# Kernel optimization log

Hardware: AMD Instinct MI355X
Metric: run time of the kernel (lower is better)

The kernel has to match this reference:

```python
import jax, jax.numpy as jnp
import numpy as np

B, L, D = 2, 1024, 768
N_LAYERS, D_STATE, D_CONV, EXPAND = 4, 16, 4, 2
D_INNER = EXPAND * D
DT_RANK = (D + 15) // 16  # 48, ceil(d_model/16) as in reference Mamba
N_CLS = 10
EPS = 1e-6


def rmsnorm(x, w):
    return x * jax.lax.rsqrt(jnp.mean(x * x, axis=-1, keepdims=True) + EPS) * w


def mamba_block(x, in_w, conv_w, conv_b, xp_w, dt_w, dt_b, A_log, D_skip, out_w):
    # x: (B, L, D)
    Bsz = x.shape[0]
    xz = jnp.einsum('bld,ed->ble', x, in_w)            # (B, L, 2*d_inner)
    xi, z = jnp.split(xz, 2, axis=-1)
    # causal depthwise conv over the sequence dim
    xc = jnp.transpose(xi, (0, 2, 1))                  # (B, d_inner, L)
    xc = jax.lax.conv_general_dilated(
        xc, conv_w[:, None, :], (1,), [(D_CONV - 1, 0)],
        dimension_numbers=('NCH', 'OIH', 'NCH'), feature_group_count=D_INNER)
    xc = jnp.transpose(xc, (0, 2, 1)) + conv_b         # (B, L, d_inner)
    xc = jax.nn.silu(xc)
    # input-dependent SSM parameters
    x_dbl = jnp.einsum('bld,ed->ble', xc, xp_w)        # (B, L, dt_rank + 2*d_state)
    dt, Bs, Cs = jnp.split(x_dbl, [DT_RANK, DT_RANK + D_STATE], axis=-1)
    delta = jax.nn.softplus(jnp.einsum('blr,dr->bld', dt, dt_w) + dt_b)  # (B, L, d_inner)
    A = -jnp.exp(A_log)                                # (d_inner, d_state)
    dA = jnp.exp(delta[..., None] * A)                 # (B, L, d_inner, d_state)
    dBu = delta[..., None] * Bs[:, :, None, :] * xc[..., None]

    def step(h, inp):
        dA_t, dBu_t, C_t = inp
        h = dA_t * h + dBu_t                           # (B, d_inner, d_state)
        y = jnp.einsum('bdn,bn->bd', h, C_t)
        return h, y

    h0 = jnp.zeros((Bsz, D_INNER, D_STATE), x.dtype)
    _, ys = jax.lax.scan(step, h0, (jnp.swapaxes(dA, 0, 1),
                                    jnp.swapaxes(dBu, 0, 1),
                                    jnp.swapaxes(Cs, 0, 1)))
    y = jnp.swapaxes(ys, 0, 1) + xc * D_skip           # (B, L, d_inner)
    y = y * jax.nn.silu(z)                             # gate
    return jnp.einsum('bld,od->blo', y, out_w)


def reference(x, norm_w, in_proj_w, conv_w, conv_b, x_proj_w, dt_proj_w, dt_proj_b,
              A_log, D_skip, out_proj_w, final_norm_w,
              head1_w, head1_b, head_norm_w, head2_w, head2_b):
    for i in range(N_LAYERS):
        res = x
        x = rmsnorm(x, norm_w[i])
        x = mamba_block(x, in_proj_w[i], conv_w[i], conv_b[i], x_proj_w[i],
                        dt_proj_w[i], dt_proj_b[i], A_log[i], D_skip[i],
                        out_proj_w[i]) + res
    x = rmsnorm(x, final_norm_w)
    last = x[:, -1, :]                                 # (B, D)
    h = last @ head1_w.T + head1_b
    h = rmsnorm(h, head_norm_w)
    h = jax.nn.gelu(h, approximate=False)              # torch nn.GELU default is exact erf
    return h @ head2_w.T + head2_b                     # (B, N_CLS)


def setup_inputs() -> dict:
    key = jax.random.key(0)
    ks = jax.random.split(key, 10)
    s = 0.02
    x = jax.random.normal(ks[0], (B, L, D), jnp.float32)
    norm_w = jnp.ones((N_LAYERS, D), jnp.float32)
    in_proj_w = s * jax.random.normal(ks[1], (N_LAYERS, 2 * D_INNER, D), jnp.float32)
    conv_w = s * jax.random.normal(ks[2], (N_LAYERS, D_INNER, D_CONV), jnp.float32)
    conv_b = jnp.zeros((N_LAYERS, D_INNER), jnp.float32)
    x_proj_w = s * jax.random.normal(ks[3], (N_LAYERS, DT_RANK + 2 * D_STATE, D_INNER), jnp.float32)
    dt_proj_w = s * jax.random.normal(ks[4], (N_LAYERS, D_INNER, DT_RANK), jnp.float32)
    dt_proj_b = jnp.full((N_LAYERS, D_INNER), -4.6, jnp.float32)  # softplus(-4.6) ~ 0.01
    A_log = jnp.log(jnp.broadcast_to(
        jnp.arange(1, D_STATE + 1, dtype=jnp.float32), (N_LAYERS, D_INNER, D_STATE)) + 0.0)
    D_skip = jnp.ones((N_LAYERS, D_INNER), jnp.float32)
    out_proj_w = s * jax.random.normal(ks[5], (N_LAYERS, D, D_INNER), jnp.float32)
    final_norm_w = jnp.ones((D,), jnp.float32)
    head1_w = s * jax.random.normal(ks[6], (D, D), jnp.float32)
    head1_b = jnp.zeros((D,), jnp.float32)
    head_norm_w = jnp.ones((D,), jnp.float32)
    head2_w = s * jax.random.normal(ks[7], (N_CLS, D), jnp.float32)
    head2_b = jnp.zeros((N_CLS,), jnp.float32)
    return {"x": x, "norm_w": norm_w, "in_proj_w": in_proj_w, "conv_w": conv_w,
            "conv_b": conv_b, "x_proj_w": x_proj_w, "dt_proj_w": dt_proj_w,
            "dt_proj_b": dt_proj_b, "A_log": A_log, "D_skip": D_skip,
            "out_proj_w": out_proj_w, "final_norm_w": final_norm_w,
            "head1_w": head1_w, "head1_b": head1_b, "head_norm_w": head_norm_w,
            "head2_w": head2_w, "head2_b": head2_b}
```

## Files before the change

kernel.cpp:

```cpp
#include <hip/hip_runtime.h>
#include <hip/hip_bf16.h>
#include <math.h>

typedef __bf16 bf16;
typedef __bf16 bf16x4 __attribute__((ext_vector_type(4)));
typedef __bf16 bf16x8 __attribute__((ext_vector_type(8)));
typedef float floatx4 __attribute__((ext_vector_type(4)));

#define BB 2
#define LL 1024
#define DD 768
#define DI 1536
#define MROWS 2048
#define NXP 80
#define DTRANK 48
#define DTPAD 64
#define DSTATE 16
#define NC 16
#define CLEN 64
#define KSPLIT 16
#define OPKS 4
#define LOG2E 1.4426950408889634f
#define LN2   0.6931471805599453f
#define TROW 132
#define SYROW 68

__device__ __forceinline__ void ld16(void* lds, const void* g) {
    __builtin_amdgcn_global_load_lds(
        (const __attribute__((address_space(1))) void*)g,
        (__attribute__((address_space(3))) void*)lds, 16, 0, 0);
}

__device__ __forceinline__ void wait_vm0() {
    asm volatile("s_waitcnt vmcnt(0)" ::: "memory");
}

__device__ __forceinline__ float row16_sum(float x) {
    float t;
    t = __int_as_float(__builtin_amdgcn_update_dpp(0, __float_as_int(x), 0x111, 0xF, 0xF, true)); x += t;
    t = __int_as_float(__builtin_amdgcn_update_dpp(0, __float_as_int(x), 0x112, 0xF, 0xF, true)); x += t;
    t = __int_as_float(__builtin_amdgcn_update_dpp(0, __float_as_int(x), 0x114, 0xF, 0xF, true)); x += t;
    t = __int_as_float(__builtin_amdgcn_update_dpp(0, __float_as_int(x), 0x118, 0xF, 0xF, true)); x += t;
    return x;
}

__device__ __forceinline__ float exp2_raw(float x) {
#if __has_builtin(__builtin_amdgcn_exp2f)
    return __builtin_amdgcn_exp2f(x);
#else
    float r; asm("v_exp_f32 %0, %1" : "=v"(r) : "v"(x)); return r;
#endif
}
__device__ __forceinline__ float log2_raw(float x) {
#if __has_builtin(__builtin_amdgcn_logf)
    return __builtin_amdgcn_logf(x);
#else
    float r; asm("v_log_f32 %0, %1" : "=v"(r) : "v"(x)); return r;
#endif
}
__device__ __forceinline__ float softplus_fast(float v) {
    float t  = exp2_raw(v * LOG2E);
    float sp = log2_raw(1.f + t) * LN2;
    return (v > 20.f) ? v : sp;
}

#define N1 (4 * 3072 * 768)
#define N2 (4 * NXP * DI)
#define N3 (4 * DI * DTPAD)
#define N4 (4 * DD * DI)
#define N5 (4 * DSTATE * DI)
__global__ __launch_bounds__(256) void cvt_all_k(const float* __restrict__ in_proj_w,
                                                 const float* __restrict__ x_proj_w,
                                                 const float* __restrict__ dt_proj_w,
                                                 const float* __restrict__ out_proj_w,
                                                 const float* __restrict__ A_log,
                                                 bf16* __restrict__ w_in,
                                                 bf16* __restrict__ w_xp,
                                                 bf16* __restrict__ w_dt,
                                                 bf16* __restrict__ w_out,
                                                 float* __restrict__ a2T) {
    int i = blockIdx.x * 256 + threadIdx.x;
    if (i < N1) { w_in[i] = (bf16)in_proj_w[i]; return; }
    i -= N1;
    if (i < N2) { w_xp[i] = (bf16)x_proj_w[i]; return; }
    i -= N2;
    if (i < N3) {
        int row = i >> 6, c = i & 63;
        w_dt[i] = (c < DTRANK) ? (bf16)dt_proj_w[row * DTRANK + c] : (bf16)0.f;
        return;
    }
    i -= N3;
    if (i < N4) { w_out[i] = (bf16)out_proj_w[i]; return; }
    i -= N4;
    if (i < N5) {
        int layer = i / (DSTATE * DI);
        int rem   = i - layer * (DSTATE * DI);
        int n     = rem / DI;
        int d     = rem - n * DI;
        a2T[i] = -__expf(A_log[(size_t)layer * DI * DSTATE + d * DSTATE + n]) * LOG2E;
    }
}

__global__ __launch_bounds__(256) void rmsnorm_k(const float* __restrict__ x,
                                                 const float* __restrict__ w,
                                                 bf16* __restrict__ out) {
    int row = blockIdx.x;
    const float* xr = x + (size_t)row * DD;
    int tid = threadIdx.x;
    float v[3]; float ss = 0.f;
    for (int j = 0; j < 3; j++) { v[j] = xr[tid + j * 256]; ss += v[j] * v[j]; }
    for (int o = 1; o < 64; o <<= 1) ss += __shfl_xor(ss, o, 64);
    __shared__ float sred[4];
    if ((tid & 63) == 0) sred[tid >> 6] = ss;
    __syncthreads();
    float scale = rsqrtf((sred[0] + sred[1] + sred[2] + sred[3]) / (float)DD + 1e-6f);
    for (int j = 0; j < 3; j++) {
        int c = tid + j * 256;
        out[(size_t)row * DD + c] = (bf16)(v[j] * scale * w[c]);
    }
}

template <int MODE>
__global__ __launch_bounds__(256) void gemm_bt(const bf16* __restrict__ A,
                                               const bf16* __restrict__ W,
                                               float* __restrict__ Cf,
                                               bf16* __restrict__ Cb,
                                               int M, int N, int K) {
    __shared__ bf16 As[128][32];
    __shared__ bf16 Ws[128][32];
    const int tid  = threadIdx.x;
    const int m0   = blockIdx.x * 128;
    const int n0   = blockIdx.y * 128;
    const int wave = tid >> 6;
    const int lane = tid & 63;
    const int wm   = (wave >> 1) * 64;
    const int wn   = (wave & 1) * 64;
    const int lrow = lane & 15;
    const int quad = lane >> 4;

    int kbeg = 0, kend = K;
    if constexpr (MODE == 5) {
        int kseg = K / gridDim.z;
        kbeg = blockIdx.z * kseg;
        kend = kbeg + kseg;
        Cf  += (size_t)blockIdx.z * M * N;
    }

    floatx4 acc[4][4];
    for (int mi = 0; mi < 4; mi++)
        for (int ni = 0; ni < 4; ni++) acc[mi][ni] = (floatx4){0.f, 0.f, 0.f, 0.f};

    const int r0  = tid >> 2;
    const int r1  = r0 + 64;
    const int seg = (tid & 3) * 8;
    char* asb0 = (char*)As + wave * 1024;
    char* asb1 = (char*)As + 4096 + wave * 1024;
    char* wsb0 = (char*)Ws + wave * 1024;
    char* wsb1 = (char*)Ws + 4096 + wave * 1024;

    for (int kb = kbeg; kb < kend; kb += 32) {
        int gk = kb + seg;
        __syncthreads();
        ld16(asb0, A + (size_t)(m0 + r0) * K + gk);
        ld16(asb1, A + (size_t)(m0 + r1) * K + gk);
        ld16(wsb0, W + (size_t)(n0 + r0) * K + gk);
        ld16(wsb1, W + (size_t)(n0 + r1) * K + gk);
        wait_vm0();
        __syncthreads();
        bf16x8 af[4], wf[4];
        for (int mi = 0; mi < 4; mi++) af[mi] = *(const bf16x8*)&As[wm + mi * 16 + lrow][quad * 8];
        for (int ni = 0; ni < 4; ni++) wf[ni] = *(const bf16x8*)&Ws[wn + ni * 16 + lrow][quad * 8];
        for (int mi = 0; mi < 4; mi++)
            for (int ni = 0; ni < 4; ni++)
                acc[mi][ni] = __builtin_amdgcn_mfma_f32_16x16x32_bf16(af[mi], wf[ni], acc[mi][ni], 0, 0, 0);
    }
    for (int mi = 0; mi < 4; mi++) {
        int rowb = m0 + wm + mi * 16 + quad * 4;
        for (int ni = 0; ni < 4; ni++) {
            int col = n0 + wn + ni * 16 + lrow;
            for (int r = 0; r < 4; r++) {
                int row = rowb + r;
                float v = acc[mi][ni][r];
                if constexpr (MODE == 1) Cb[(size_t)row * N + col] = (bf16)v;
                else                     Cf[(size_t)row * N + col] = v;
            }
        }
    }
}

__global__ __launch_bounds__(256) void op_reduce_norm_k(const float* __restrict__ part,
                                                        const float* __restrict__ resid,
                                                        const float* __restrict__ nw,
                                                        float* __restrict__ xout,
                                                        bf16* __restrict__ xnb) {
    int row = blockIdx.x;
    int tid = threadIdx.x;
    float v[3]; float ss = 0.f;
    for (int j = 0; j < 3; j++) {
        int c = tid + j * 256;
        size_t idx = (size_t)row * DD + c;
        float s = resid[idx];
        for (int ks = 0; ks < OPKS; ks++) s += part[(size_t)ks * MROWS * DD + idx];
        v[j] = s;
        xout[idx] = s;
        ss += s * s;
    }
    for (int o = 1; o < 64; o <<= 1) ss += __shfl_xor(ss, o, 64);
    __shared__ float sred[4];
    if ((tid & 63) == 0) sred[tid >> 6] = ss;
    __syncthreads();
    float scale = rsqrtf((sred[0] + sred[1] + sred[2] + sred[3]) / (float)DD + 1e-6f);
    for (int j = 0; j < 3; j++) {
        int c = tid + j * 256;
        xnb[(size_t)row * DD + c] = (bf16)(v[j] * scale * nw[c]);
    }
}

__global__ __launch_bounds__(256) void gemm_xp(const bf16* __restrict__ A,
                                               const bf16* __restrict__ W,
                                               float* __restrict__ part) {
    __shared__ bf16 As[64][40];
    __shared__ bf16 Ws[128][40];
    const int tid  = threadIdx.x;
    const int m0   = blockIdx.x * 64;
    const int ks   = blockIdx.y;
    const int k0   = ks * (DI / KSPLIT);
    const int wave = tid >> 6;
    const int lane = tid & 63;
    const int lrow = lane & 15;
    const int quad = lane >> 4;
    const int wm   = wave * 16;

    floatx4 acc[5];
    for (int ni = 0; ni < 5; ni++) acc[ni] = (floatx4){0.f, 0.f, 0.f, 0.f};

    const int ra  = tid >> 2;
    const int rw1 = ra + 64;
    const int seg = (tid & 3) * 8;

    for (int kb = 0; kb < DI / KSPLIT; kb += 32) {
        int gk = k0 + kb + seg;
        bf16x8 va = *(const bf16x8*)(A + (size_t)(m0 + ra) * DI + gk);
        bf16x8 vw0, vw1;
        if (ra < NXP) vw0 = *(const bf16x8*)(W + (size_t)ra * DI + gk);
        else          for (int j = 0; j < 8; j++) vw0[j] = (bf16)0.f;
        if (rw1 < NXP) vw1 = *(const bf16x8*)(W + (size_t)rw1 * DI + gk);
        else           for (int j = 0; j < 8; j++) vw1[j] = (bf16)0.f;
        __syncthreads();
        *(bf16x8*)&As[ra][seg]  = va;
        *(bf16x8*)&Ws[ra][seg]  = vw0;
        *(bf16x8*)&Ws[rw1][seg] = vw1;
        __syncthreads();
        bf16x8 af = *(const bf16x8*)&As[wm + lrow][quad * 8];
        for (int ni = 0; ni < 5; ni++) {
            bf16x8 wf = *(const bf16x8*)&Ws[ni * 16 + lrow][quad * 8];
            acc[ni] = __builtin_amdgcn_mfma_f32_16x16x32_bf16(af, wf, acc[ni], 0, 0, 0);
        }
    }
    float* pout = part + (size_t)ks * MROWS * NXP;
    for (int ni = 0; ni < 5; ni++) {
        int col = ni * 16 + lrow;
        for (int r = 0; r < 4; r++) {
            int row = m0 + wm + quad * 4 + r;
            pout[(size_t)row * NXP + col] = acc[ni][r];
        }
    }
}

__global__ __launch_bounds__(256) void xp_reduce_k(const float* __restrict__ part,
                                                   float* __restrict__ xdbl,
                                                   bf16* __restrict__ dtbf) {
    int idx = blockIdx.x * 256 + threadIdx.x;
    if (idx >= MROWS * NXP) return;
    float s = 0.f;
    for (int j = 0; j < KSPLIT; j++) s += part[(size_t)j * MROWS * NXP + idx];
    xdbl[idx] = s;
    int m = idx / NXP, c = idx - m * NXP;
    if (c < DTRANK)      dtbf[m * DTPAD + c] = (bf16)s;
    else if (c < DTPAD)  dtbf[m * DTPAD + c] = (bf16)0.f;
}

__global__ __launch_bounds__(256) void conv_silu_k(const bf16* __restrict__ xz,
                                                   const float* __restrict__ cw,
                                                   const float* __restrict__ cb,
                                                   bf16* __restrict__ xcb,
                                                   bf16* __restrict__ gzb) {
    int t = blockIdx.x * 256 + threadIdx.x;
    if (t >= MROWS * (DI / 4)) return;
    int m = t / (DI / 4);
    int d = (t - m * (DI / 4)) * 4;
    int l = m & (LL - 1);
    float acc[4];
    floatx4 cwv[4];
    for (int q = 0; q < 4; q++) {
        acc[q] = cb[d + q];
        cwv[q] = *(const floatx4*)&cw[(d + q) * 4];
    }
    for (int k = 0; k < 4; k++) {
        int lp = l - 3 + k;
        if (lp >= 0) {
            bf16x4 v = *(const bf16x4*)&xz[(size_t)(m - 3 + k) * (2 * DI) + d];
            for (int q = 0; q < 4; q++) acc[q] += (float)v[q] * cwv[q][k];
        }
    }
    bf16x4 xo, go;
    bf16x4 z4 = *(const bf16x4*)&xz[(size_t)m * (2 * DI) + DI + d];
    for (int q = 0; q < 4; q++) {
        float s = acc[q] / (1.f + __expf(-acc[q]));
        xo[q] = (bf16)s;
        float zv = (float)z4[q];
        go[q] = (bf16)(zv / (1.f + __expf(-zv)));
    }
    *(bf16x4*)&xcb[(size_t)m * DI + d] = xo;
    *(bf16x4*)&gzb[(size_t)m * DI + d] = go;
}

__global__ __launch_bounds__(256) void scanA_k(const bf16* __restrict__ dtb,
                                               const bf16* __restrict__ wdt,
                                               const float* __restrict__ dtbias,
                                               const bf16* __restrict__ xcb,
                                               const float* __restrict__ xdbl,
                                               const float* __restrict__ A_log,
                                               float* __restrict__ Pbuf,
                                               float* __restrict__ Sbuf,
                                               float2* __restrict__ ylsc) {
    const int b   = blockIdx.y;
    const int d0  = blockIdx.x * 16;
    const int c   = blockIdx.z;
    const int tid = threadIdx.x;
    const int dl  = tid >> 4;
    const int n   = tid & 15;
    const int wv  = tid >> 6;
    const int lane = tid & 63;
    const int lr  = lane & 15;
    const int q   = lane >> 4;
    const int l0  = c * CLEN;

    const float a2 = -__expf(A_log[(size_t)(d0 + dl) * DSTATE + n]) * LOG2E;
    const float bi = dtbias[d0 + lr];

    __shared__ __align__(16) bf16  sxc[CLEN][16];
    __shared__ __align__(16) float sdpT[16][TROW];
    __shared__ __align__(16) float sbcT[16][TROW];
    __shared__ __align__(16) float syT[16][SYROW];
    __shared__ __align__(16) float sST[16][SYROW];

    const bf16x8 wf0 = *(const bf16x8*)&wdt[(size_t)(d0 + lr) * DTPAD + q * 8];
    const bf16x8 wf1 = *(const bf16x8*)&wdt[(size_t)(d0 + lr) * DTPAD + 32 + q * 8];

    bf16x8 a0, a1;
    {
        const bf16* r = &dtb[(size_t)(b * LL + l0 + 16 * wv + lr) * DTPAD + q * 8];
        a0 = *(const bf16x8*)r;
        a1 = *(const bf16x8*)(r + 32);
    }
    float Bv[4], Cv[4];
    #pragma unroll
    for (int k2 = 0; k2 < 4; ++k2) {
        int ii = (tid + 256 * k2) >> 4;
        const float* p = &xdbl[(size_t)(b * LL + l0 + ii) * NXP + DTRANK + n];
        Bv[k2] = p[0];
        Cv[k2] = p[DSTATE];
    }
    if (tid < 128) {
        int r2 = tid >> 1, c2 = tid & 1;
        ld16((char*)&sxc[0][0] + (tid & ~63) * 16,
             xcb + (size_t)(b * LL + l0 + r2) * DI + d0 + c2 * 8);
    }
    wait_vm0();
    __syncthreads();

    {
        floatx4 dacc = (floatx4){0.f, 0.f, 0.f, 0.f};
        dacc = __builtin_amdgcn_mfma_f32_16x16x32_bf16(a0, wf0, dacc, 0, 0, 0);
        dacc = __builtin_amdgcn_mfma_f32_16x16x32_bf16(a1, wf1, dacc, 0, 0, 0);
        float vv[4], xvv[4];
        #pragma unroll
        for (int r = 0; r < 4; ++r) {
            int l = 16 * wv + q * 4 + r;
            vv[r]  = softplus_fast(dacc[r] + bi);
            xvv[r] = (float)sxc[l][lr];
        }
        int L0 = 16 * wv + q * 4;
        *(float4*)&sdpT[lr][2 * L0] =
            make_float4(vv[0], vv[0] * xvv[0], vv[1], vv[1] * xvv[1]);
        *(float4*)&sdpT[lr][2 * L0 + 4] =
            make_float4(vv[2], vv[2] * xvv[2], vv[3], vv[3] * xvv[3]);
        #pragma unroll
        for (int k2 = 0; k2 < 4; ++k2) {
            int ii = (tid + 256 * k2) >> 4;
            *(float2*)&sbcT[n][2 * ii] = make_float2(Bv[k2], Cv[k2]);
        }
    }
    __syncthreads();

    {
        float h = 0.f, sdc = 0.f;
        const float4* dpr = (const float4*)&sdpT[dl][0];
        const float4* bcr = (const float4*)&sbcT[n][0];
        float4 dA[4], bA[4], dB2[4], bB2[4];
        float y4[4], s4[4];
        #pragma unroll
        for (int t = 0; t < 4; ++t) { dA[t] = dpr[t]; bA[t] = bcr[t]; }
        #pragma unroll
        for (int g = 0; g < 8; ++g) {
            #pragma unroll
            for (int t = 0; t < 4; ++t) {
                if (g + 1 < 8) {
                    if ((g & 1) == 0) { dB2[t] = dpr[(g + 1) * 4 + t]; bB2[t] = bcr[(g + 1) * 4 + t]; }
                    else              { dA[t]  = dpr[(g + 1) * 4 + t]; bA[t]  = bcr[(g + 1) * 4 + t]; }
                }
            }
            #pragma unroll
            for (int i = 0; i < 8; ++i) {
                float4 v = ((g & 1) == 0) ? dA[i >> 1] : dB2[i >> 1];
                float4 w = ((g & 1) == 0) ? bA[i >> 1] : bB2[i >> 1];
                float dvx = (i & 1) ? v.z : v.x;
                float dpy = (i & 1) ? v.w : v.y;
                float bx  = (i & 1) ? w.z : w.x;
                float cy  = (i & 1) ? w.w : w.y;
                float e = exp2_raw(dvx * a2);
                h = __builtin_fmaf(e, h, dpy * bx);
                sdc += dvx;
                y4[i & 3] = row16_sum(h * cy);
                s4[i & 3] = sdc;
                if ((i & 3) == 3 && n == 0) {
                    *(floatx4*)&syT[dl][g * 8 + i - 3] =
                        (floatx4){y4[0], y4[1], y4[2], y4[3]};
                    *(floatx4*)&sST[dl][g * 8 + i - 3] =
                        (floatx4){s4[0], s4[1], s4[2], s4[3]};
                }
            }
        }
        size_t o = (((size_t)c * BB + b) * DI + (d0 + dl)) * DSTATE + n;
        Pbuf[o] = exp2_raw(a2 * sdc);
        Sbuf[o] = h;
    }
    __syncthreads();

    #pragma unroll
    for (int k2 = 0; k2 < 4; ++k2) {
        int idx = tid + 256 * k2, ii = idx >> 4, dd = idx & 15;
        ylsc[(size_t)(b * LL + l0 + ii) * DI + d0 + dd] =
            make_float2(syT[dd][ii], sST[dd][ii]);
    }
}

__global__ __launch_bounds__(256) void compose_k(const float* __restrict__ P,
                                                 const float* __restrict__ S,
                                                 float* __restrict__ H0T) {
    int idx = blockIdx.x * 256 + threadIdx.x;
    const size_t stride = (size_t)BB * DI * DSTATE;
    int b = idx / (DI * DSTATE);
    int rest = idx - b * (DI * DSTATE);
    int d = rest >> 4;
    int n = rest & 15;
    float h = 0.f;
    #pragma unroll
    for (int c = 0; c < NC; ++c) {
        H0T[((size_t)c * BB + b) * (DSTATE * DI) + (size_t)n * DI + d] = h;
        h = __builtin_fmaf(P[(size_t)c * stride + idx], h, S[(size_t)c * stride + idx]);
    }
}

__global__ __launch_bounds__(256) void corr_k(const float2* __restrict__ ylsc,
                                              const float* __restrict__ xdbl,
                                              const float* __restrict__ H0T,
                                              const float* __restrict__ a2T,
                                              const bf16* __restrict__ xcb,
                                              const bf16* __restrict__ gzb,
                                              const float* __restrict__ Dskip,
                                              bf16* __restrict__ ybf) {
    const int b = blockIdx.y, c = blockIdx.z;
    const int tid = threadIdx.x;
    const int t6 = blockIdx.x * 256 + tid;
    const int dq   = (t6 % 384) * 4;
    const int loff = t6 / 384;

    __shared__ __align__(16) float sC[CLEN][16];
    {
        int l = tid >> 2, nn = (tid & 3) * 4;
        *(float4*)&sC[l][nn] =
            *(const float4*)&xdbl[(size_t)(b * LL + c * CLEN + l) * NXP + DTRANK + DSTATE + nn];
    }
    __syncthreads();

    const float* h0base = H0T + ((size_t)c * BB + b) * (DSTATE * DI);
    int m0_ = b * LL + c * CLEN + loff;
    floatx4 acc[4];
    float4 sc[4];
    #pragma unroll
    for (int s = 0; s < 4; ++s) {
        size_t mo = (size_t)(m0_ + s * 16) * DI + dq;
        float4 u0 = *(const float4*)&ylsc[mo];
        float4 u1 = *(const float4*)&ylsc[mo + 2];
        acc[s] = (floatx4){u0.x, u0.z, u1.x, u1.z};
        sc[s]  = make_float4(u0.y, u0.w, u1.y, u1.w);
    }
    #pragma unroll
    for (int n = 0; n < DSTATE; ++n) {
        float4 a2v = *(const float4*)&a2T[(size_t)n * DI + dq];
        float4 h0v = *(const float4*)&h0base[(size_t)n * DI + dq];
        #pragma unroll
        for (int s = 0; s < 4; ++s) {
            float Cn = sC[loff + s * 16][n];
            acc[s][0] = __builtin_fmaf(Cn * h0v.x, exp2_raw(a2v.x * sc[s].x), acc[s][0]);
            acc[s][1] = __builtin_fmaf(Cn * h0v.y, exp2_raw(a2v.y * sc[s].y), acc[s][1]);
            acc[s][2] = __builtin_fmaf(Cn * h0v.z, exp2_raw(a2v.z * sc[s].z), acc[s][2]);
            acc[s][3] = __builtin_fmaf(Cn * h0v.w, exp2_raw(a2v.w * sc[s].w), acc[s][3]);
        }
    }
    float4 Dsk = *(const float4*)&Dskip[dq];
    #pragma unroll
    for (int s = 0; s < 4; ++s) {
        size_t mo = (size_t)(m0_ + s * 16) * DI + dq;
        bf16x4 xc4 = *(const bf16x4*)&xcb[mo];
        bf16x4 gz4 = *(const bf16x4*)&gzb[mo];
        bf16x4 yo;
        yo[0] = (bf16)((acc[s][0] + (float)xc4[0] * Dsk.x) * (float)gz4[0]);
        yo[1] = (bf16)((acc[s][1] + (float)xc4[1] * Dsk.y) * (float)gz4[1]);
        yo[2] = (bf16)((acc[s][2] + (float)xc4[2] * Dsk.z) * (float)gz4[2]);
        yo[3] = (bf16)((acc[s][3] + (float)xc4[3] * Dsk.w) * (float)gz4[3]);
        *(bf16x4*)&ybf[mo] = yo;
    }
}

__global__ __launch_bounds__(256) void head_norm_k(const float* __restrict__ x,
                                                   const float* __restrict__ fnw,
                                                   float* __restrict__ xn_buf) {
    int b = blockIdx.x;
    int tid = threadIdx.x;
    const float* xr = x + ((size_t)b * LL + (LL - 1)) * DD;
    __shared__ float sred[4];
    float v[3]; float ss = 0.f;
    for (int j = 0; j < 3; j++) { v[j] = xr[tid + j * 256]; ss += v[j] * v[j]; }
    for (int o = 1; o < 64; o <<= 1) ss += __shfl_xor(ss, o, 64);
    if ((tid & 63) == 0) sred[tid >> 6] = ss;
    __syncthreads();
    float scale = rsqrtf((sred[0] + sred[1] + sred[2] + sred[3]) / (float)DD + 1e-6f);
    for (int j = 0; j < 3; j++) {
        int c = tid + j * 256;
        xn_buf[(size_t)b * DD + c] = v[j] * scale * fnw[c];
    }
}

__global__ __launch_bounds__(256) void head_h1_k(const float* __restrict__ xn_buf,
                                                 const float* __restrict__ h1w,
                                                 const float* __restrict__ h1b,
                                                 float* __restrict__ h_buf) {
    int b  = blockIdx.x;
    int o0 = blockIdx.y * 64;
    int tid = threadIdx.x;
    __shared__ float sx[DD];
    for (int c = tid; c < DD; c += 256) sx[c] = xn_buf[(size_t)b * DD + c];
    __syncthreads();
    int wave = tid >> 6, lane = tid & 63;
    for (int j = 0; j < 16; j++) {
        int o = o0 + wave * 16 + j;
        const float* wrow = h1w + (size_t)o * DD;
        float acc = 0.f;
        for (int k = 0; k < 12; k++) {
            int c = lane + 64 * k;
            acc += wrow[c] * sx[c];
        }
        for (int off = 1; off < 64; off <<= 1) acc += __shfl_xor(acc, off, 64);
        if (lane == 0) h_buf[(size_t)b * DD + o] = acc + h1b[o];
    }
}

__global__ __launch_bounds__(256) void head_out_k(const float* __restrict__ h_buf,
                                                  const float* __restrict__ hnw,
                                                  const float* __restrict__ h2w,
                                                  const float* __restrict__ h2b,
                                                  float* __restrict__ out) {
    int b = blockIdx.x;
    int tid = threadIdx.x;
    __shared__ float hh[DD];
    __shared__ float sred[4];
    const float* hr = h_buf + (size_t)b * DD;
    float ss = 0.f;
    for (int c = tid; c < DD; c += 256) { float v = hr[c]; ss += v * v; }
    for (int o = 1; o < 64; o <<= 1) ss += __shfl_xor(ss, o, 64);
    if ((tid & 63) == 0) sred[tid >> 6] = ss;
    __syncthreads();
    float sc = rsqrtf((sred[0] + sred[1] + sred[2] + sred[3]) / (float)DD + 1e-6f);
    for (int c = tid; c < DD; c += 256) {
        float v = hr[c] * sc * hnw[c];
        hh[c] = 0.5f * v * (1.f + erff(v * 0.70710678118f));
    }
    __syncthreads();
    int w = tid >> 6, lane = tid & 63;
    for (int j = w; j < 10; j += 4) {
        float acc = 0.f;
        const float* wrow = h2w + (size_t)j * DD;
        for (int c = lane; c < DD; c += 64) acc += hh[c] * wrow[c];
        for (int o = 1; o < 64; o <<= 1) acc += __shfl_xor(acc, o, 64);
        if (lane == 0) out[b * 10 + j] = acc + h2b[j];
    }
}

extern "C" void kernel_launch(void* const* d_in, const int* in_sizes, int n_in,
                              void* d_out, int out_size, void* d_ws, size_t ws_size,
                              hipStream_t stream) {
    const float* x_in      = (const float*)d_in[0];
    const float* norm_w    = (const float*)d_in[1];
    const float* in_proj_w = (const float*)d_in[2];
    const float* conv_w    = (const float*)d_in[3];
    const float* conv_b    = (const float*)d_in[4];
    const float* x_proj_w  = (const float*)d_in[5];
    const float* dt_proj_w = (const float*)d_in[6];
    const float* dt_proj_b = (const float*)d_in[7];
    const float* A_log     = (const float*)d_in[8];
    const float* D_skip    = (const float*)d_in[9];
    const float* out_proj_w= (const float*)d_in[10];
    const float* fnw       = (const float*)d_in[11];
    const float* h1w       = (const float*)d_in[12];
    const float* h1b       = (const float*)d_in[13];
    const float* hnw       = (const float*)d_in[14];
    const float* h2w       = (const float*)d_in[15];
    const float* h2b       = (const float*)d_in[16];
    float* out = (float*)d_out;

    char* ws = (char*)d_ws;
    size_t off = 0;
    auto alloc = [&](size_t bytes) -> void* {
        void* p = ws + off;
        off += (bytes + 255) & ~(size_t)255;
        return p;
    };
    bf16* w_in  = (bf16*)alloc((size_t)N1 * 2);
    bf16* w_xp  = (bf16*)alloc((size_t)N2 * 2);
    bf16* w_dt  = (bf16*)alloc((size_t)N3 * 2);
    bf16* w_out = (bf16*)alloc((size_t)N4 * 2);
    float* a2T  = (float*)alloc((size_t)N5 * 4);
    bf16* xn_bf = (bf16*)alloc((size_t)MROWS * DD * 2);
    bf16* xz_bf = (bf16*)alloc((size_t)MROWS * 2 * DI * 2);
    bf16* xc_bf = (bf16*)alloc((size_t)MROWS * DI * 2);
    bf16* gz_bf = (bf16*)alloc((size_t)MROWS * DI * 2);
    float* xdbl = (float*)alloc((size_t)MROWS * NXP * 4);
    bf16* dt_bf = (bf16*)alloc((size_t)MROWS * DTPAD * 2);
    bf16* y_bf  = (bf16*)alloc((size_t)MROWS * DI * 2);
    float* x_buf= (float*)alloc((size_t)MROWS * DD * 4);
    float* Pbuf = (float*)alloc((size_t)NC * BB * DI * DSTATE * 4);
    float* Sbuf = (float*)alloc((size_t)NC * BB * DI * DSTATE * 4);
    float* H0T  = (float*)alloc((size_t)NC * BB * DI * DSTATE * 4);
    float2* ylsc= (float2*)alloc((size_t)MROWS * DI * 8);
    float* xnl  = (float*)alloc((size_t)BB * DD * 4);
    float* hbuf = (float*)alloc((size_t)BB * DD * 4);
    float* xp_part = (float*)alloc((size_t)KSPLIT * MROWS * NXP * 4);
    float* op_part = (float*)alloc((size_t)OPKS * MROWS * DD * 4);

    {
        int ntot = N1 + N2 + N3 + N4 + N5;
        cvt_all_k<<<(ntot + 255) / 256, 256, 0, stream>>>(
            in_proj_w, x_proj_w, dt_proj_w, out_proj_w, A_log,
            w_in, w_xp, w_dt, w_out, a2T);
    }

    for (int i = 0; i < 4; i++) {
        const float* x_src = (i == 0) ? x_in : x_buf;
        if (i == 0)
            rmsnorm_k<<<MROWS, 256, 0, stream>>>(x_src, norm_w, xn_bf);
        gemm_bt<1><<<dim3(MROWS / 128, 3072 / 128), 256, 0, stream>>>(
            xn_bf, w_in + (size_t)i * 3072 * 768, nullptr, xz_bf,
            MROWS, 2 * DI, DD);
        conv_silu_k<<<(MROWS * (DI / 4) + 255) / 256, 256, 0, stream>>>(
            xz_bf, conv_w + (size_t)i * DI * 4, conv_b + (size_t)i * DI, xc_bf, gz_bf);
        gemm_xp<<<dim3(MROWS / 64, KSPLIT), 256, 0, stream>>>(
            xc_bf, w_xp + (size_t)i * NXP * DI, xp_part);
        xp_reduce_k<<<(MROWS * NXP + 255) / 256, 256, 0, stream>>>(xp_part, xdbl, dt_bf);
        scanA_k<<<dim3(DI / 16, BB, NC), 256, 0, stream>>>(
            dt_bf, w_dt + (size_t)i * DI * DTPAD, dt_proj_b + (size_t)i * DI,
            xc_bf, xdbl, A_log + (size_t)i * DI * DSTATE, Pbuf, Sbuf, ylsc);
        compose_k<<<(BB * DI * DSTATE) / 256, 256, 0, stream>>>(Pbuf, Sbuf, H0T);
        corr_k<<<dim3(24, BB, NC), 256, 0, stream>>>(
            ylsc, xdbl, H0T, a2T + (size_t)i * DSTATE * DI,
            xc_bf, gz_bf, D_skip + (size_t)i * DI, y_bf);
        gemm_bt<5><<<dim3(MROWS / 128, DD / 128, OPKS), 256, 0, stream>>>(
            y_bf, w_out + (size_t)i * DD * DI, op_part, nullptr,
            MROWS, DD, DI);
        op_reduce_norm_k<<<MROWS, 256, 0, stream>>>(
            op_part, x_src, norm_w + ((i + 1) & 3) * DD, x_buf, xn_bf);
    }

    head_norm_k<<<BB, 256, 0, stream>>>(x_buf, fnw, xnl);
    head_h1_k<<<dim3(BB, DD / 64), 256, 0, stream>>>(xnl, h1w, h1b, hbuf);
    head_out_k<<<BB, 256, 0, stream>>>(hbuf, hnw, h2w, h2b, out);
}
```

Baseline: 626.5 us.

## Restructure chunked scan so each thread owns four states of 64-channel block

The chunk-scan kernel now handles 64 channels per block instead of 16. Each thread keeps four state elements in registers, so the per-step reduction over states needs two DPP shuffles instead of four. The dt projection runs four MFMA tiles per block, and the per-step results are written straight to global memory, which removes the transposed LDS staging and one barrier. The cost is a quarter as many blocks (fewer waves to hide latency), four exp2 calls per thread per step, and scattered 8-byte global stores from one lane in four.

```diff
diff --git a/kernel.cpp b/kernel.cpp
--- a/kernel.cpp
+++ b/kernel.cpp
@@ -18,12 +18,11 @@
 #define DSTATE 16
 #define NC 16
 #define CLEN 64
+#define DBLK 64
 #define KSPLIT 16
 #define OPKS 4
 #define LOG2E 1.4426950408889634f
 #define LN2   0.6931471805599453f
-#define TROW 132
-#define SYROW 68
 
 __device__ __forceinline__ void ld16(void* lds, const void* g) {
     __builtin_amdgcn_global_load_lds(
@@ -35,12 +34,10 @@
     asm volatile("s_waitcnt vmcnt(0)" ::: "memory");
 }
 
-__device__ __forceinline__ float row16_sum(float x) {
+__device__ __forceinline__ float quad4_sum(float x) {
     float t;
-    t = __int_as_float(__builtin_amdgcn_update_dpp(0, __float_as_int(x), 0x111, 0xF, 0xF, true)); x += t;
-    t = __int_as_float(__builtin_amdgcn_update_dpp(0, __float_as_int(x), 0x112, 0xF, 0xF, true)); x += t;
-    t = __int_as_float(__builtin_amdgcn_update_dpp(0, __float_as_int(x), 0x114, 0xF, 0xF, true)); x += t;
-    t = __int_as_float(__builtin_amdgcn_update_dpp(0, __float_as_int(x), 0x118, 0xF, 0xF, true)); x += t;
+    t = __int_as_float(__builtin_amdgcn_update_dpp(0, __float_as_int(x), 0xB1, 0xF, 0xF, true)); x += t;
+    t = __int_as_float(__builtin_amdgcn_update_dpp(0, __float_as_int(x), 0x4E, 0xF, 0xF, true)); x += t;
     return x;
 }
 
@@ -315,7 +312,7 @@
     *(bf16x4*)&gzb[(size_t)m * DI + d] = go;
 }
 
-__global__ __launch_bounds__(256) void scanA_k(const bf16* __restrict__ dtb,
+__global__ __launch_bounds__(256) void scanB_k(const bf16* __restrict__ dtb,
                                                const bf16* __restrict__ wdt,
                                                const float* __restrict__ dtbias,
                                                const bf16* __restrict__ xcb,
@@ -325,124 +322,124 @@
                                                float* __restrict__ Sbuf,
                                                float2* __restrict__ ylsc) {
     const int b   = blockIdx.y;
-    const int d0  = blockIdx.x * 16;
+    const int d0  = blockIdx.x * DBLK;
     const int c   = blockIdx.z;
     const int tid = threadIdx.x;
-    const int dl  = tid >> 4;
-    const int n   = tid & 15;
     const int wv  = tid >> 6;
     const int lane = tid & 63;
     const int lr  = lane & 15;
     const int q   = lane >> 4;
     const int l0  = c * CLEN;
-
-    const float a2 = -__expf(A_log[(size_t)(d0 + dl) * DSTATE + n]) * LOG2E;
-    const float bi = dtbias[d0 + lr];
-
-    __shared__ __align__(16) bf16  sxc[CLEN][16];
-    __shared__ __align__(16) float sdpT[16][TROW];
-    __shared__ __align__(16) float sbcT[16][TROW];
-    __shared__ __align__(16) float syT[16][SYROW];
-    __shared__ __align__(16) float sST[16][SYROW];
-
-    const bf16x8 wf0 = *(const bf16x8*)&wdt[(size_t)(d0 + lr) * DTPAD + q * 8];
-    const bf16x8 wf1 = *(const bf16x8*)&wdt[(size_t)(d0 + lr) * DTPAD + 32 + q * 8];
-
-    bf16x8 a0, a1;
+    const int dl  = tid >> 2;
+    const int nq  = tid & 3;
+
+    __shared__ __align__(16) float sdp[DBLK][68];
+    __shared__ __align__(16) bf16  sxc[CLEN][DBLK];
+    __shared__ __align__(16) float sB[CLEN][20];
+    __shared__ __align__(16) float sC[CLEN][20];
+
     {
-        const bf16* r = &dtb[(size_t)(b * LL + l0 + 16 * wv + lr) * DTPAD + q * 8];
-        a0 = *(const bf16x8*)r;
-        a1 = *(const bf16x8*)(r + 32);
-    }
-    float Bv[4], Cv[4];
-    #pragma unroll
-    for (int k2 = 0; k2 < 4; ++k2) {
-        int ii = (tid + 256 * k2) >> 4;
-        const float* p = &xdbl[(size_t)(b * LL + l0 + ii) * NXP + DTRANK + n];
-        Bv[k2] = p[0];
-        Cv[k2] = p[DSTATE];
-    }
-    if (tid < 128) {
-        int r2 = tid >> 1, c2 = tid & 1;
-        ld16((char*)&sxc[0][0] + (tid & ~63) * 16,
-             xcb + (size_t)(b * LL + l0 + r2) * DI + d0 + c2 * 8);
-    }
-    wait_vm0();
-    __syncthreads();
+        int t2 = tid;
+        ld16((char*)&sxc[0][0] + (t2 & ~63) * 16,
+             xcb + (size_t)(b * LL + l0 + (t2 >> 3)) * DI + d0 + (t2 & 7) * 8);
+        t2 = tid + 256;
+        ld16((char*)&sxc[0][0] + (t2 & ~63) * 16,
+             xcb + (size_t)(b * LL + l0 + (t2 >> 3)) * DI + d0 + (t2 & 7) * 8);
+    }
 
     {
-        floatx4 dacc = (floatx4){0.f, 0.f, 0.f, 0.f};
-        dacc = __builtin_amdgcn_mfma_f32_16x16x32_bf16(a0, wf0, dacc, 0, 0, 0);
-        dacc = __builtin_amdgcn_mfma_f32_16x16x32_bf16(a1, wf1, dacc, 0, 0, 0);
-        float vv[4], xvv[4];
-        #pragma unroll
-        for (int r = 0; r < 4; ++r) {
-            int l = 16 * wv + q * 4 + r;
-            vv[r]  = softplus_fast(dacc[r] + bi);
-            xvv[r] = (float)sxc[l][lr];
-        }
-        int L0 = 16 * wv + q * 4;
-        *(float4*)&sdpT[lr][2 * L0] =
-            make_float4(vv[0], vv[0] * xvv[0], vv[1], vv[1] * xvv[1]);
-        *(float4*)&sdpT[lr][2 * L0 + 4] =
-            make_float4(vv[2], vv[2] * xvv[2], vv[3], vv[3] * xvv[3]);
+        float Bv[4], Cv[4];
         #pragma unroll
         for (int k2 = 0; k2 < 4; ++k2) {
             int ii = (tid + 256 * k2) >> 4;
-            *(float2*)&sbcT[n][2 * ii] = make_float2(Bv[k2], Cv[k2]);
-        }
-    }
-    __syncthreads();
-
+            const float* p = &xdbl[(size_t)(b * LL + l0 + ii) * NXP + DTRANK + (tid & 15)];
+            Bv[k2] = p[0];
+            Cv[k2] = p[DSTATE];
+        }
+        #pragma unroll
+        for (int k2 = 0; k2 < 4; ++k2) {
+            int ii = (tid + 256 * k2) >> 4;
+            sB[ii][tid & 15] = Bv[k2];
+            sC[ii][tid & 15] = Cv[k2];
+        }
+    }
+
+    float4 a2q;
     {
-        float h = 0.f, sdc = 0.f;
-        const float4* dpr = (const float4*)&sdpT[dl][0];
-        const float4* bcr = (const float4*)&sbcT[n][0];
-        float4 dA[4], bA[4], dB2[4], bB2[4];
-        float y4[4], s4[4];
+        float4 al = *(const float4*)&A_log[(size_t)(d0 + dl) * DSTATE + nq * 4];
+        a2q.x = -__expf(al.x) * LOG2E;
+        a2q.y = -__expf(al.y) * LOG2E;
+        a2q.z = -__expf(al.z) * LOG2E;
+        a2q.w = -__expf(al.w) * LOG2E;
+    }
+
+    {
+        const bf16* ar = &dtb[(size_t)(b * LL + l0 + 16 * wv + lr) * DTPAD + q * 8];
+        bf16x8 a0 = *(const bf16x8*)ar;
+        bf16x8 a1 = *(const bf16x8*)(ar + 32);
         #pragma unroll
-        for (int t = 0; t < 4; ++t) { dA[t] = dpr[t]; bA[t] = bcr[t]; }
-        #pragma unroll
-        for (int g = 0; g < 8; ++g) {
+        for (int j = 0; j < 4; ++j) {
+            const bf16* wr = &wdt[(size_t)(d0 + 16 * j + lr) * DTPAD + q * 8];
+            bf16x8 w0 = *(const bf16x8*)wr;
+            bf16x8 w1 = *(const bf16x8*)(wr + 32);
+            floatx4 dacc = (floatx4){0.f, 0.f, 0.f, 0.f};
+            dacc = __builtin_amdgcn_mfma_f32_16x16x32_bf16(a0, w0, dacc, 0, 0, 0);
+            dacc = __builtin_amdgcn_mfma_f32_16x16x32_bf16(a1, w1, dacc, 0, 0, 0);
+            float bi = dtbias[d0 + 16 * j + lr];
             #pragma unroll
-            for (int t = 0; t < 4; ++t) {
-                if (g + 1 < 8) {
-                    if ((g & 1) == 0) { dB2[t] = dpr[(g + 1) * 4 + t]; bB2[t] = bcr[(g + 1) * 4 + t]; }
-                    else              { dA[t]  = dpr[(g + 1) * 4 + t]; bA[t]  = bcr[(g + 1) * 4 + t]; }
-                }
+            for (int r = 0; r < 4; ++r) {
+                int l = 16 * wv + q * 4 + r;
+                sdp[16 * j + lr][l] = softplus_fast(dacc[r] + bi);
             }
+        }
+    }
+
+    wait_vm0();
+    __syncthreads();
+
+    {
+        float4 hq = make_float4(0.f, 0.f, 0.f, 0.f);
+        float sdc = 0.f;
+        const float* dvrow = &sdp[dl][0];
+        const unsigned short* xcp = (const unsigned short*)&sxc[0][0] + dl;
+        for (int g = 0; g < 16; ++g) {
+            float4 dvv = *(const float4*)&dvrow[4 * g];
+            float2 yst[4];
             #pragma unroll
-            for (int i = 0; i < 8; ++i) {
-                float4 v = ((g & 1) == 0) ? dA[i >> 1] : dB2[i >> 1];
-                float4 w = ((g & 1) == 0) ? bA[i >> 1] : bB2[i >> 1];
-                float dvx = (i & 1) ? v.z : v.x;
-                float dpy = (i & 1) ? v.w : v.y;
-                float bx  = (i & 1) ? w.z : w.x;
-                float cy  = (i & 1) ? w.w : w.y;
-                float e = exp2_raw(dvx * a2);
-                h = __builtin_fmaf(e, h, dpy * bx);
-                sdc += dvx;
-                y4[i & 3] = row16_sum(h * cy);
-                s4[i & 3] = sdc;
-                if ((i & 3) == 3 && n == 0) {
-                    *(floatx4*)&syT[dl][g * 8 + i - 3] =
-                        (floatx4){y4[0], y4[1], y4[2], y4[3]};
-                    *(floatx4*)&sST[dl][g * 8 + i - 3] =
-                        (floatx4){s4[0], s4[1], s4[2], s4[3]};
-                }
+            for (int i2 = 0; i2 < 4; ++i2) {
+                int i = 4 * g + i2;
+                float dv = (i2 == 0) ? dvv.x : (i2 == 1) ? dvv.y : (i2 == 2) ? dvv.z : dvv.w;
+                float xcv = __int_as_float((unsigned)xcp[i * DBLK] << 16);
+                float du = dv * xcv;
+                float4 Bq = *(const float4*)&sB[i][4 * nq];
+                float4 Cq = *(const float4*)&sC[i][4 * nq];
+                hq.x = __builtin_fmaf(exp2_raw(a2q.x * dv), hq.x, du * Bq.x);
+                hq.y = __builtin_fmaf(exp2_raw(a2q.y * dv), hq.y, du * Bq.y);
+                hq.z = __builtin_fmaf(exp2_raw(a2q.z * dv), hq.z, du * Bq.z);
+                hq.w = __builtin_fmaf(exp2_raw(a2q.w * dv), hq.w, du * Bq.w);
+                float y = __builtin_fmaf(Cq.w, hq.w,
+                          __builtin_fmaf(Cq.z, hq.z,
+                          __builtin_fmaf(Cq.y, hq.y, Cq.x * hq.x)));
+                y = quad4_sum(y);
+                sdc += dv;
+                yst[i2] = make_float2(y, sdc);
             }
-        }
-        size_t o = (((size_t)c * BB + b) * DI + (d0 + dl)) * DSTATE + n;
-        Pbuf[o] = exp2_raw(a2 * sdc);
-        Sbuf[o] = h;
-    }
-    __syncthreads();
-
-    #pragma unroll
-    for (int k2 = 0; k2 < 4; ++k2) {
-        int idx = tid + 256 * k2, ii = idx >> 4, dd = idx & 15;
-        ylsc[(size_t)(b * LL + l0 + ii) * DI + d0 + dd] =
-            make_float2(syT[dd][ii], sST[dd][ii]);
+            if (nq == 0) {
+                size_t base = (size_t)(b * LL + l0 + 4 * g) * DI + d0 + dl;
+                ylsc[base]          = yst[0];
+                ylsc[base + DI]     = yst[1];
+                ylsc[base + 2 * DI] = yst[2];
+                ylsc[base + 3 * DI] = yst[3];
+            }
+        }
+        float4 Pq;
+        Pq.x = exp2_raw(a2q.x * sdc);
+        Pq.y = exp2_raw(a2q.y * sdc);
+        Pq.z = exp2_raw(a2q.z * sdc);
+        Pq.w = exp2_raw(a2q.w * sdc);
+        size_t o = (((size_t)c * BB + b) * DI + (d0 + dl)) * DSTATE + nq * 4;
+        *(float4*)&Pbuf[o] = Pq;
+        *(float4*)&Sbuf[o] = make_float4(hq.x, hq.y, hq.z, hq.w);
     }
 }
 
@@ -669,7 +666,7 @@
         gemm_xp<<<dim3(MROWS / 64, KSPLIT), 256, 0, stream>>>(
             xc_bf, w_xp + (size_t)i * NXP * DI, xp_part);
         xp_reduce_k<<<(MROWS * NXP + 255) / 256, 256, 0, stream>>>(xp_part, xdbl, dt_bf);
-        scanA_k<<<dim3(DI / 16, BB, NC), 256, 0, stream>>>(
+        scanB_k<<<dim3(DI / DBLK, BB, NC), 256, 0, stream>>>(
             dt_bf, w_dt + (size_t)i * DI * DTPAD, dt_proj_b + (size_t)i * DI,
             xc_bf, xdbl, A_log + (size_t)i * DI * DSTATE, Pbuf, Sbuf, ylsc);
         compose_k<<<(BB * DI * DSTATE) / 256, 256, 0, stream>>>(Pbuf, Sbuf, H0T);
```

Measured after the change: 595.1 us. -5.0%, faster.
